# Kernel tuning notes

Hardware: AMD Instinct MI355X
Metric: run time of the kernel (lower is better)

Reference implementation:

```python
import jax, jax.numpy as jnp
import numpy as np

MASK_VALUE = -1000000.0  # matches torch sequence_mask fill value


def setup_inputs() -> dict:
    key = jax.random.key(0)
    k1, k2, k3, k4 = jax.random.split(key, 4)
    B, Tq, Tk, d = 16, 2048, 2048, 128
    queries = jax.random.normal(k1, (B, Tq, d), dtype=jnp.float32)
    keys = jax.random.normal(k2, (B, Tk, d), dtype=jnp.float32)
    values = jax.random.normal(k3, (B, Tk, d), dtype=jnp.float32)
    valid_lens = jax.random.randint(k4, (B, Tq), 0, Tk, dtype=jnp.int64)
    return {"queries": queries, "keys": keys, "values": values,
            "valid_lens": valid_lens}


def reference(queries, keys, values, valid_lens):
    d = queries.shape[-1]
    Tk = keys.shape[1]
    # scores: [B, Tq, Tk]
    scores = jnp.einsum('bqd,bkd->bqk', queries, keys) / jnp.sqrt(
        jnp.asarray(d, dtype=queries.dtype))
    # per-row length mask: position k is valid iff k < valid_lens[b, q]
    mask = jnp.arange(Tk)[None, None, :] < valid_lens[:, :, None]
    scores = jnp.where(mask, scores, jnp.asarray(MASK_VALUE, scores.dtype))
    attn = jax.nn.softmax(scores, axis=-1)
    # dropout p=0.0 -> identity
    return jnp.einsum('bqk,bkd->bqd', attn, values)
```

## Files before the change

kernel.cpp:

```cpp
#include <hip/hip_runtime.h>
#include <stdint.h>
#include <math.h>

#define NB 16
#define TQ 2048
#define TK 2048
#define DH 128
#define KT (TK / 64)
#define QB (TQ / 64)

#define CT   8
#define CTL  3
#define NCH  4
#define NJOBS (NB * QB * NCH)
#define PBLK 768

#define QK_STR 136
#define VT_STR 72
#define P_STR  72

#define SK_OFF 0
#define SV_OFF 17408
#define SP_OFF 35840
#define SM_BYTES 45056

typedef __attribute__((ext_vector_type(8))) short bf16x8;
typedef __attribute__((ext_vector_type(4))) float f32x4;
typedef __attribute__((ext_vector_type(8))) unsigned short u16x8;

__device__ __forceinline__ unsigned short f2b(float f) {
  union { float f; uint32_t u; } v; v.f = f;
  uint32_t u = v.u;
  return (unsigned short)((u + 0x7fffu + ((u >> 16) & 1u)) >> 16);
}

__device__ __forceinline__ u16x8 cvt8(const float* p) {
  const f32x4 a = *(const f32x4*)p;
  const f32x4 b = *(const f32x4*)(p + 4);
  u16x8 o;
#pragma unroll
  for (int j = 0; j < 4; ++j) { o[j] = f2b(a[j]); o[4 + j] = f2b(b[j]); }
  return o;
}

__device__ __forceinline__ int eff_len(const int* vlen, bool is64, int idx) {
  int v = is64 ? vlen[2 * idx] : vlen[idx];
  v = (v < 0) ? 0 : ((v > TK) ? TK : v);
  return (v == 0) ? TK : v;
}

__global__ __launch_bounds__(256) void prep_sort(const float* __restrict__ K,
                                                 const float* __restrict__ V,
                                                 unsigned short* __restrict__ Kb,
                                                 unsigned short* __restrict__ Vt,
                                                 const int* __restrict__ vlen,
                                                 int* __restrict__ perm,
                                                 int* __restrict__ tick) {
  __shared__ alignas(16) char sm[17424];
  const int t = threadIdx.x;
  const int b = blockIdx.y;

  if (blockIdx.x == KT) {
    int* cnt_  = (int*)sm;
    int* base_ = cnt_ + (TK + 1);
    int* psum  = base_ + (TK + 1);

    if (b == 0 && t == 0) tick[0] = 0;

    int hw = 0;
#pragma unroll
    for (int i = 0; i < 8; ++i) hw |= vlen[2 * i + 1];
    const bool is64 = (hw == 0);

    for (int i = t; i <= TK; i += 256) cnt_[i] = 0;
    __syncthreads();

    int eff[8];
#pragma unroll
    for (int j = 0; j < 8; ++j) {
      const int q = j * 256 + t;
      eff[j] = eff_len(vlen, is64, b * TQ + q);
      atomicAdd(&cnt_[eff[j]], 1);
    }
    __syncthreads();

    int loc[8]; int s = 0;
#pragma unroll
    for (int j = 0; j < 8; ++j) { loc[j] = cnt_[TK - (t * 8 + j)]; s += loc[j]; }
    psum[t] = s;
    __syncthreads();
    if (t == 0) {
      int acc = 0;
      for (int i = 0; i < 256; ++i) { const int x = psum[i]; psum[i] = acc; acc += x; }
    }
    __syncthreads();
    int run = psum[t];
#pragma unroll
    for (int j = 0; j < 8; ++j) { base_[TK - (t * 8 + j)] = run; run += loc[j]; }
    __syncthreads();
#pragma unroll
    for (int j = 0; j < 8; ++j) {
      const int rank = atomicAdd(&base_[eff[j]], 1);
      perm[b * TQ + rank] = j * 256 + t;
    }
    return;
  }

  unsigned short (*tile)[136] = (unsigned short (*)[136])sm;
  const int kt = blockIdx.x;
  const int k0 = kt * 64;

  const float* Ks = K + ((size_t)b * TK + k0) * DH;
  unsigned short* Kd = Kb + ((size_t)b * TK + k0) * DH;
#pragma unroll
  for (int i = 0; i < 4; ++i) {
    const int row = i * 16 + (t >> 4);
    const int c0 = (t & 15) * 8;
    *(u16x8*)(Kd + (size_t)row * DH + c0) = cvt8(Ks + (size_t)row * DH + c0);
  }
  const float* Vs = V + ((size_t)b * TK + k0) * DH;
#pragma unroll
  for (int i = 0; i < 4; ++i) {
    const int row = i * 16 + (t >> 4);
    const int c0 = (t & 15) * 8;
    *(u16x8*)(&tile[row][c0]) = cvt8(Vs + (size_t)row * DH + c0);
  }
  __syncthreads();
  {
    const int d = t >> 1;
    const int half = t & 1;
    alignas(16) unsigned short tmp[32];
#pragma unroll
    for (int j = 0; j < 32; ++j) tmp[j] = tile[half * 32 + j][d];
    unsigned short* dst = Vt + ((size_t)(b * KT + kt) * DH + d) * 64 + half * 32;
#pragma unroll
    for (int j = 0; j < 4; ++j)
      *(u16x8*)(dst + j * 8) = *(const u16x8*)(&tmp[j * 8]);
  }
}

__global__ __launch_bounds__(256) void attn_pers(const float* __restrict__ Q,
                                                 const unsigned short* __restrict__ Kp,
                                                 const unsigned short* __restrict__ Vp,
                                                 const int* __restrict__ vlen,
                                                 const int* __restrict__ perm,
                                                 float* __restrict__ pO,
                                                 float* __restrict__ pL,
                                                 float* __restrict__ out,
                                                 int* __restrict__ tick) {
  __shared__ alignas(16) char smem[SM_BYTES];
  __shared__ int s_job;
  unsigned short* sK = (unsigned short*)(smem + SK_OFF);
  unsigned short* sV = (unsigned short*)(smem + SV_OFF);

  const int tid  = threadIdx.x;
  const int w    = tid >> 6;
  const int lane = tid & 63;
  const int quad = lane >> 4;
  const int l15  = lane & 15;
  const int krow = tid >> 4;
  const int kch  = tid & 15;

  int hw = 0;
#pragma unroll
  for (int i = 0; i < 8; ++i) hw |= vlen[2 * i + 1];
  const bool is64 = (hw == 0);

  const float kScaleL2 = 0.08838834764831845f * 1.4426950408889634f;
  const float kBias    = -32.0f;
  const float kKill    = -1.0e7f;

  unsigned short* sP = (unsigned short*)(smem + SP_OFF) + w * (16 * P_STR);

  for (;;) {
    __syncthreads();
    if (tid == 0) s_job = atomicAdd(tick, 1);
    __syncthreads();
    const int job = s_job;
    if (job >= NJOBS) return;

    const int cchunk = job >> 9;
    const int jq     = (job >> 4) & 31;
    const int b      = job & 15;
    const int q0 = jq * 64;
    const int qw = q0 + w * 16;

    const int bvl = eff_len(vlen, is64, b * TQ + perm[b * TQ + q0]);
    const int wvl = eff_len(vlen, is64, b * TQ + perm[b * TQ + qw]);
    const int nt = (bvl + 63) >> 6;
    const int t0 = cchunk * CT;
    const int t1 = (nt < t0 + CT) ? nt : (t0 + CT);
    if (t0 >= t1) continue;
    const int nact = (nt + CT - 1) >> CTL;

    const unsigned short* Kbase = Kp + (size_t)b * TK * DH;
    const unsigned short* Vbase = Vp + (size_t)(b * KT) * DH * 64;

    u16x8 kreg[4], vreg[4];
    {
      const unsigned short* Ksrc = Kbase + (size_t)t0 * 64 * DH;
#pragma unroll
      for (int i = 0; i < 4; ++i)
        kreg[i] = *(const u16x8*)(Ksrc + (size_t)(i * 16 + krow) * DH + kch * 8);
      const unsigned short* Vsrc = Vbase + (size_t)t0 * (DH * 64);
#pragma unroll
      for (int i = 0; i < 4; ++i)
        vreg[i] = *(const u16x8*)(Vsrc + (i * 256 + tid) * 8);
    }

    bf16x8 qa[4];
    {
      const int qmrow = perm[b * TQ + qw + l15];
      const float* qptr = Q + ((size_t)b * TQ + qmrow) * DH + quad * 8;
#pragma unroll
      for (int kc = 0; kc < 4; ++kc) {
        union { u16x8 u; bf16x8 f; } cv;
        cv.u = cvt8(qptr + kc * 32);
        qa[kc] = cv.f;
      }
    }

    int vlr[4]; float scl[4]; int qidx[4];
#pragma unroll
    for (int r = 0; r < 4; ++r) {
      const int rank = qw + quad * 4 + r;
      const int qrow = perm[b * TQ + rank];
      qidx[r] = qrow;
      const int idx = b * TQ + qrow;
      int v = is64 ? vlen[2 * idx] : vlen[idx];
      v = (v < 0) ? 0 : ((v > TK) ? TK : v);
      scl[r] = (v == 0) ? 0.0f : kScaleL2;
      vlr[r] = (v == 0) ? TK : v;
    }

    f32x4 Of[8] = {};
    float l_r[4] = {0.f, 0.f, 0.f, 0.f};

    for (int t = t0; t < t1; ++t) {
#pragma unroll
      for (int i = 0; i < 4; ++i)
        *(u16x8*)(sK + (i * 16 + krow) * QK_STR + kch * 8) = kreg[i];
#pragma unroll
      for (int i = 0; i < 4; ++i) {
        const int chunk = i * 256 + tid;
        *(u16x8*)(sV + (chunk >> 3) * VT_STR + (chunk & 7) * 8) = vreg[i];
      }
      __syncthreads();

      if (t + 1 < t1) {
        const unsigned short* Ksrc = Kbase + (size_t)(t + 1) * 64 * DH;
#pragma unroll
        for (int i = 0; i < 4; ++i)
          kreg[i] = *(const u16x8*)(Ksrc + (size_t)(i * 16 + krow) * DH + kch * 8);
        const unsigned short* Vsrc = Vbase + (size_t)(t + 1) * (DH * 64);
#pragma unroll
        for (int i = 0; i < 4; ++i)
          vreg[i] = *(const u16x8*)(Vsrc + (i * 256 + tid) * 8);
      }

      const int k0 = t * 64;
      if (k0 < wvl) {
        f32x4 sc[4] = {};
#pragma unroll
        for (int ct = 0; ct < 4; ++ct) {
          const unsigned short* kr = sK + (ct * 16 + l15) * QK_STR;
#pragma unroll
          for (int kc = 0; kc < 4; ++kc) {
            const bf16x8 kf = *(const bf16x8*)(kr + (kc * 4 + quad) * 8);
            sc[ct] = __builtin_amdgcn_mfma_f32_16x16x32_bf16(qa[kc], kf, sc[ct], 0, 0, 0);
          }
        }

        unsigned short pb[4][4];
#pragma unroll
        for (int ct = 0; ct < 4; ++ct) {
          const int kpos = k0 + ct * 16 + l15;
#pragma unroll
          for (int r = 0; r < 4; ++r) {
            const float s = (kpos < vlr[r]) ? fmaf(sc[ct][r], scl[r], kBias) : kKill;
            const float p = exp2f(s);
            l_r[r] += p;
            pb[ct][r] = f2b(p);
          }
        }

#pragma unroll
        for (int ct = 0; ct < 4; ++ct)
#pragma unroll
          for (int r = 0; r < 4; ++r)
            sP[(quad * 4 + r) * P_STR + ct * 16 + l15] = pb[ct][r];
        __asm__ __volatile__("" ::: "memory");

        bf16x8 pa[2];
        {
          const unsigned short* pr = sP + l15 * P_STR;
#pragma unroll
          for (int ch = 0; ch < 2; ++ch)
            pa[ch] = *(const bf16x8*)(pr + (ch * 4 + quad) * 8);
        }

#pragma unroll
        for (int dt = 0; dt < 8; ++dt) {
          const unsigned short* vr = sV + (dt * 16 + l15) * VT_STR;
#pragma unroll
          for (int ch = 0; ch < 2; ++ch) {
            const bf16x8 vf = *(const bf16x8*)(vr + (ch * 4 + quad) * 8);
            Of[dt] = __builtin_amdgcn_mfma_f32_16x16x32_bf16(pa[ch], vf, Of[dt], 0, 0, 0);
          }
        }
      }
      __syncthreads();
    }

#pragma unroll
    for (int off = 1; off <= 8; off <<= 1)
#pragma unroll
      for (int r = 0; r < 4; ++r)
        l_r[r] += __shfl_xor(l_r[r], off, 64);

    if (nact == 1) {
#pragma unroll
      for (int r = 0; r < 4; ++r) {
        const float inv = 1.0f / l_r[r];
        float* orow = out + ((size_t)b * TQ + qidx[r]) * DH;
#pragma unroll
        for (int dt = 0; dt < 8; ++dt)
          orow[dt * 16 + l15] = Of[dt][r] * inv;
      }
      continue;
    }

    const int slot = (b * QB + jq) * NCH + cchunk;
    float* po = pO + (size_t)slot * (64 * DH);
    float* pl = pL + (size_t)slot * 64;
#pragma unroll
    for (int r = 0; r < 4; ++r) {
      const int row = w * 16 + quad * 4 + r;
#pragma unroll
      for (int dt = 0; dt < 8; ++dt)
        po[(size_t)row * DH + dt * 16 + l15] = Of[dt][r];
    }
    if (l15 == 0) {
#pragma unroll
      for (int r = 0; r < 4; ++r)
        pl[w * 16 + quad * 4 + r] = l_r[r];
    }
  }
}

__global__ __launch_bounds__(256) void combine_kernel(const float* __restrict__ pO,
                                                      const float* __restrict__ pL,
                                                      const int* __restrict__ perm,
                                                      const int* __restrict__ vlen,
                                                      float* __restrict__ out) {
  const int b = blockIdx.y;
  const int j = blockIdx.x;
  const int t = threadIdx.x;

  int hw = 0;
#pragma unroll
  for (int i = 0; i < 8; ++i) hw |= vlen[2 * i + 1];
  const bool is64 = (hw == 0);

  const int bvl = eff_len(vlen, is64, b * TQ + perm[b * TQ + j * 64]);
  const int nt = (bvl + 63) >> 6;
  const int nact = (nt + CT - 1) >> CTL;
  if (nact <= 1) return;

  const int qboff = (b * QB + j) * NCH;
#pragma unroll
  for (int i = 0; i < 8; ++i) {
    const int u = i * 256 + t;
    const int r = u >> 5;
    const int d4 = (u & 31) * 4;
    float lsum = 0.0f;
    f32x4 acc = {0.f, 0.f, 0.f, 0.f};
    for (int c = 0; c < nact; ++c) {
      lsum += pL[(size_t)(qboff + c) * 64 + r];
      acc += *(const f32x4*)(pO + ((size_t)(qboff + c) * 64 + r) * DH + d4);
    }
    const float inv = 1.0f / lsum;
    const int qi = perm[b * TQ + j * 64 + r];
    *(f32x4*)(out + ((size_t)b * TQ + qi) * DH + d4) = acc * inv;
  }
}

__global__ __launch_bounds__(256) void attn_fb(const float* __restrict__ Q,
                                               const float* __restrict__ Kp,
                                               const float* __restrict__ Vp,
                                               const int* __restrict__ vlen,
                                               float* __restrict__ out) {
  __shared__ alignas(16) char smem[53248];
  __shared__ int s_bvl[4];
  unsigned short* sQ = (unsigned short*)smem;
  unsigned short* sK = (unsigned short*)(smem + 17408);
  unsigned short* sV = (unsigned short*)(smem + 34816);

  const int tid  = threadIdx.x;
  const int w    = tid >> 6;
  const int lane = tid & 63;
  const int quad = lane >> 4;
  const int l15  = lane & 15;
  const int b    = blockIdx.y;
  const int q0   = blockIdx.x * 64;

  const float* Qb = Q + ((size_t)b * TQ + q0) * DH;
#pragma unroll
  for (int i = 0; i < 4; ++i) {
    const int row = i * 16 + (tid >> 4);
    const int c0 = (tid & 15) * 8;
    *(u16x8*)(sQ + row * QK_STR + c0) = cvt8(Qb + (size_t)row * DH + c0);
  }

  int hw = 0;
#pragma unroll
  for (int i = 0; i < 8; ++i) hw |= vlen[2 * i + 1];
  const bool is64 = (hw == 0);

  const float kScaleL2 = 0.08838834764831845f * 1.4426950408889634f;
  const float kBias    = -32.0f;
  const float kKill    = -1.0e7f;

  const int qw = q0 + w * 16;
  int vlr[4];
  float scl[4];
#pragma unroll
  for (int r = 0; r < 4; ++r) {
    const int idx = b * TQ + qw + quad * 4 + r;
    int v = is64 ? vlen[2 * idx] : vlen[idx];
    v = (v < 0) ? 0 : ((v > TK) ? TK : v);
    scl[r] = (v == 0) ? 0.0f : kScaleL2;
    vlr[r] = (v == 0) ? TK : v;
  }
  int wvl = 0;
#pragma unroll
  for (int r = 0; r < 4; ++r) wvl = max(wvl, vlr[r]);
  wvl = max(wvl, __shfl_xor(wvl, 16, 64));
  wvl = max(wvl, __shfl_xor(wvl, 32, 64));
  if (lane == 0) s_bvl[w] = wvl;
  __syncthreads();
  const int bvl = max(max(s_bvl[0], s_bvl[1]), max(s_bvl[2], s_bvl[3]));
  const int nt = (bvl + 63) >> 6;

  bf16x8 qa[4];
  {
    const unsigned short* qrow = sQ + (w * 16 + l15) * QK_STR;
#pragma unroll
    for (int kc = 0; kc < 4; ++kc)
      qa[kc] = *(const bf16x8*)(qrow + (kc * 4 + quad) * 8);
  }
  unsigned short* sP = (unsigned short*)smem + w * (16 * P_STR);

  f32x4 Of[8] = {};
  float l_r[4] = {0.f, 0.f, 0.f, 0.f};

  const float* Kb = Kp + (size_t)b * TK * DH;
  const float* Vb = Vp + (size_t)b * TK * DH;

  for (int t = 0; t < nt; ++t) {
    const int k0 = t * 64;
    __syncthreads();
#pragma unroll
    for (int i = 0; i < 4; ++i) {
      const int row = i * 16 + (tid >> 4);
      const int c0 = (tid & 15) * 8;
      *(u16x8*)(sK + row * QK_STR + c0) = cvt8(Kb + (size_t)(k0 + row) * DH + c0);
    }
#pragma unroll
    for (int i = 0; i < 4; ++i) {
      const int row = i * 16 + (tid >> 4);
      const int c0 = (tid & 15) * 8;
      *(u16x8*)(sV + row * QK_STR + c0) = cvt8(Vb + (size_t)(k0 + row) * DH + c0);
    }
    __syncthreads();
    if (k0 >= wvl) continue;

    f32x4 sc[4] = {};
#pragma unroll
    for (int ct = 0; ct < 4; ++ct) {
      const unsigned short* kr = sK + (ct * 16 + l15) * QK_STR;
#pragma unroll
      for (int kc = 0; kc < 4; ++kc) {
        const bf16x8 kf = *(const bf16x8*)(kr + (kc * 4 + quad) * 8);
        sc[ct] = __builtin_amdgcn_mfma_f32_16x16x32_bf16(qa[kc], kf, sc[ct], 0, 0, 0);
      }
    }
    unsigned short pb[4][4];
#pragma unroll
    for (int ct = 0; ct < 4; ++ct) {
      const int kpos = k0 + ct * 16 + l15;
#pragma unroll
      for (int r = 0; r < 4; ++r) {
        const float s = (kpos < vlr[r]) ? fmaf(sc[ct][r], scl[r], kBias) : kKill;
        const float p = exp2f(s);
        l_r[r] += p;
        pb[ct][r] = f2b(p);
      }
    }
#pragma unroll
    for (int ct = 0; ct < 4; ++ct)
#pragma unroll
      for (int r = 0; r < 4; ++r)
        sP[(quad * 4 + r) * P_STR + ct * 16 + l15] = pb[ct][r];
    __asm__ __volatile__("" ::: "memory");
    bf16x8 pa[2];
    {
      const unsigned short* pr = sP + l15 * P_STR;
#pragma unroll
      for (int ch = 0; ch < 2; ++ch)
        pa[ch] = *(const bf16x8*)(pr + (ch * 4 + quad) * 8);
    }
#pragma unroll
    for (int dt = 0; dt < 8; ++dt) {
      const int col = dt * 16 + l15;
#pragma unroll
      for (int ch = 0; ch < 2; ++ch) {
        bf16x8 vf;
#pragma unroll
        for (int j = 0; j < 8; ++j) {
          const int k = ch * 32 + quad * 8 + j;
          vf[j] = ((const short*)sV)[k * QK_STR + col];
        }
        Of[dt] = __builtin_amdgcn_mfma_f32_16x16x32_bf16(pa[ch], vf, Of[dt], 0, 0, 0);
      }
    }
  }

#pragma unroll
  for (int off = 1; off <= 8; off <<= 1)
#pragma unroll
    for (int r = 0; r < 4; ++r)
      l_r[r] += __shfl_xor(l_r[r], off, 64);

#pragma unroll
  for (int r = 0; r < 4; ++r) {
    const float inv = 1.0f / l_r[r];
    const int q = qw + quad * 4 + r;
    float* orow = out + ((size_t)b * TQ + q) * DH;
#pragma unroll
    for (int dt = 0; dt < 8; ++dt)
      orow[dt * 16 + l15] = Of[dt][r] * inv;
  }
}

extern "C" void kernel_launch(void* const* d_in, const int* in_sizes, int n_in,
                              void* d_out, int out_size, void* d_ws, size_t ws_size,
                              hipStream_t stream) {
  const float* Q = (const float*)d_in[0];
  const float* K = (const float*)d_in[1];
  const float* V = (const float*)d_in[2];
  const int* vl  = (const int*)d_in[3];
  float* out     = (float*)d_out;

  const size_t kb    = (size_t)NB * TK * DH;
  const size_t kvB   = kb * 2 * 2;
  const size_t permB = (size_t)NB * TQ * sizeof(int);
  const size_t tickB = 256;
  const size_t pLB   = (size_t)NB * QB * NCH * 64 * sizeof(float);
  const size_t pOB   = (size_t)NB * QB * NCH * 64 * DH * sizeof(float);

  if (ws_size >= kvB + permB + tickB + pLB + pOB) {
    unsigned short* Kb = (unsigned short*)d_ws;
    unsigned short* Vt = Kb + kb;
    int*   perm = (int*)((char*)d_ws + kvB);
    int*   tick = (int*)((char*)d_ws + kvB + permB);
    float* pL   = (float*)((char*)d_ws + kvB + permB + tickB);
    float* pO   = (float*)((char*)d_ws + kvB + permB + tickB + pLB);
    prep_sort<<<dim3(KT + 1, NB), 256, 0, stream>>>(K, V, Kb, Vt, vl, perm, tick);
    attn_pers<<<dim3(PBLK), 256, 0, stream>>>(Q, Kb, Vt, vl, perm, pO, pL, out, tick);
    combine_kernel<<<dim3(QB, NB), 256, 0, stream>>>(pO, pL, perm, vl, out);
  } else {
    attn_fb<<<dim3(QB, NB), 256, 0, stream>>>(Q, K, V, vl, out);
  }
}
```

Baseline: 180.3 us.

## Process 128 query rows per job so each wave reuses K/V tiles twice

Doubles the query tile per persistent job from 64 to 128 rows, so each wave handles two 16-row groups. Every K and V fragment read from shared memory now feeds two MFMAs, and each staged K/V tile serves twice as many queries, halving global K/V traffic per query. It also adds s_setprio around the MFMA loops, reduces the persistent grid to 512 blocks, and resizes the combine kernel and partial buffers to match. The cost is higher register pressure from doubled accumulators, fewer jobs for load balancing across the sorted variable-length rows, and coarser length skipping within a 128-row block.

```diff
diff --git a/kernel.cpp b/kernel.cpp
--- a/kernel.cpp
+++ b/kernel.cpp
@@ -9,11 +9,13 @@
 #define KT (TK / 64)
 #define QB (TQ / 64)
 
+#define QBLK 128
+#define QBn  (TQ / QBLK)
 #define CT   8
 #define CTL  3
 #define NCH  4
-#define NJOBS (NB * QB * NCH)
-#define PBLK 768
+#define NJOBS (NB * QBn * NCH)
+#define PBLK 512
 
 #define QK_STR 136
 #define VT_STR 72
@@ -22,7 +24,7 @@
 #define SK_OFF 0
 #define SV_OFF 17408
 #define SP_OFF 35840
-#define SM_BYTES 45056
+#define SM_BYTES 54272
 
 typedef __attribute__((ext_vector_type(8))) short bf16x8;
 typedef __attribute__((ext_vector_type(4))) float f32x4;
@@ -170,7 +172,7 @@
   const float kBias    = -32.0f;
   const float kKill    = -1.0e7f;
 
-  unsigned short* sP = (unsigned short*)(smem + SP_OFF) + w * (16 * P_STR);
+  unsigned short* sP = (unsigned short*)(smem + SP_OFF) + w * (32 * P_STR);
 
   for (;;) {
     __syncthreads();
@@ -179,11 +181,11 @@
     const int job = s_job;
     if (job >= NJOBS) return;
 
-    const int cchunk = job >> 9;
-    const int jq     = (job >> 4) & 31;
+    const int cchunk = job >> 8;
+    const int jq     = (job >> 4) & 15;
     const int b      = job & 15;
-    const int q0 = jq * 64;
-    const int qw = q0 + w * 16;
+    const int q0 = jq * QBLK;
+    const int qw = q0 + w * 32;
 
     const int bvl = eff_len(vlen, is64, b * TQ + perm[b * TQ + q0]);
     const int wvl = eff_len(vlen, is64, b * TQ + perm[b * TQ + qw]);
@@ -208,33 +210,34 @@
         vreg[i] = *(const u16x8*)(Vsrc + (i * 256 + tid) * 8);
     }
 
-    bf16x8 qa[4];
-    {
-      const int qmrow = perm[b * TQ + qw + l15];
+    bf16x8 qa[2][4];
+#pragma unroll
+    for (int rh = 0; rh < 2; ++rh) {
+      const int qmrow = perm[b * TQ + qw + rh * 16 + l15];
       const float* qptr = Q + ((size_t)b * TQ + qmrow) * DH + quad * 8;
 #pragma unroll
       for (int kc = 0; kc < 4; ++kc) {
         union { u16x8 u; bf16x8 f; } cv;
         cv.u = cvt8(qptr + kc * 32);
-        qa[kc] = cv.f;
-      }
-    }
-
-    int vlr[4]; float scl[4]; int qidx[4];
-#pragma unroll
-    for (int r = 0; r < 4; ++r) {
-      const int rank = qw + quad * 4 + r;
-      const int qrow = perm[b * TQ + rank];
-      qidx[r] = qrow;
-      const int idx = b * TQ + qrow;
-      int v = is64 ? vlen[2 * idx] : vlen[idx];
-      v = (v < 0) ? 0 : ((v > TK) ? TK : v);
-      scl[r] = (v == 0) ? 0.0f : kScaleL2;
-      vlr[r] = (v == 0) ? TK : v;
-    }
-
-    f32x4 Of[8] = {};
-    float l_r[4] = {0.f, 0.f, 0.f, 0.f};
+        qa[rh][kc] = cv.f;
+      }
+    }
+
+    int vlr[2][4]; float scl[2][4];
+#pragma unroll
+    for (int rh = 0; rh < 2; ++rh)
+#pragma unroll
+      for (int r = 0; r < 4; ++r) {
+        const int rank = qw + rh * 16 + quad * 4 + r;
+        const int idx = b * TQ + perm[b * TQ + rank];
+        int v = is64 ? vlen[2 * idx] : vlen[idx];
+        v = (v < 0) ? 0 : ((v > TK) ? TK : v);
+        scl[rh][r] = (v == 0) ? 0.0f : kScaleL2;
+        vlr[rh][r] = (v == 0) ? TK : v;
+      }
+
+    f32x4 Of[2][8] = {};
+    float l_r[2][4] = {};
 
     for (int t = t0; t < t1; ++t) {
 #pragma unroll
@@ -260,90 +263,108 @@
 
       const int k0 = t * 64;
       if (k0 < wvl) {
-        f32x4 sc[4] = {};
+        f32x4 sc[2][4] = {};
+        __builtin_amdgcn_s_setprio(1);
 #pragma unroll
         for (int ct = 0; ct < 4; ++ct) {
           const unsigned short* kr = sK + (ct * 16 + l15) * QK_STR;
 #pragma unroll
           for (int kc = 0; kc < 4; ++kc) {
             const bf16x8 kf = *(const bf16x8*)(kr + (kc * 4 + quad) * 8);
-            sc[ct] = __builtin_amdgcn_mfma_f32_16x16x32_bf16(qa[kc], kf, sc[ct], 0, 0, 0);
+            sc[0][ct] = __builtin_amdgcn_mfma_f32_16x16x32_bf16(qa[0][kc], kf, sc[0][ct], 0, 0, 0);
+            sc[1][ct] = __builtin_amdgcn_mfma_f32_16x16x32_bf16(qa[1][kc], kf, sc[1][ct], 0, 0, 0);
           }
         }
-
-        unsigned short pb[4][4];
-#pragma unroll
-        for (int ct = 0; ct < 4; ++ct) {
-          const int kpos = k0 + ct * 16 + l15;
-#pragma unroll
-          for (int r = 0; r < 4; ++r) {
-            const float s = (kpos < vlr[r]) ? fmaf(sc[ct][r], scl[r], kBias) : kKill;
-            const float p = exp2f(s);
-            l_r[r] += p;
-            pb[ct][r] = f2b(p);
+        __builtin_amdgcn_s_setprio(0);
+
+#pragma unroll
+        for (int rh = 0; rh < 2; ++rh) {
+          unsigned short pb[4][4];
+#pragma unroll
+          for (int ct = 0; ct < 4; ++ct) {
+            const int kpos = k0 + ct * 16 + l15;
+#pragma unroll
+            for (int r = 0; r < 4; ++r) {
+              const float s = (kpos < vlr[rh][r]) ? fmaf(sc[rh][ct][r], scl[rh][r], kBias) : kKill;
+              const float p = exp2f(s);
+              l_r[rh][r] += p;
+              pb[ct][r] = f2b(p);
+            }
+          }
+#pragma unroll
+          for (int ct = 0; ct < 4; ++ct)
+#pragma unroll
+            for (int r = 0; r < 4; ++r)
+              sP[(rh * 16 + quad * 4 + r) * P_STR + ct * 16 + l15] = pb[ct][r];
+        }
+        __asm__ __volatile__("" ::: "memory");
+
+        bf16x8 pa[2][2];
+#pragma unroll
+        for (int rh = 0; rh < 2; ++rh) {
+          const unsigned short* pr = sP + (rh * 16 + l15) * P_STR;
+#pragma unroll
+          for (int ch = 0; ch < 2; ++ch)
+            pa[rh][ch] = *(const bf16x8*)(pr + (ch * 4 + quad) * 8);
+        }
+
+        __builtin_amdgcn_s_setprio(1);
+#pragma unroll
+        for (int dt = 0; dt < 8; ++dt) {
+          const unsigned short* vr = sV + (dt * 16 + l15) * VT_STR;
+#pragma unroll
+          for (int ch = 0; ch < 2; ++ch) {
+            const bf16x8 vf = *(const bf16x8*)(vr + (ch * 4 + quad) * 8);
+            Of[0][dt] = __builtin_amdgcn_mfma_f32_16x16x32_bf16(pa[0][ch], vf, Of[0][dt], 0, 0, 0);
+            Of[1][dt] = __builtin_amdgcn_mfma_f32_16x16x32_bf16(pa[1][ch], vf, Of[1][dt], 0, 0, 0);
           }
         }
-
-#pragma unroll
-        for (int ct = 0; ct < 4; ++ct)
-#pragma unroll
-          for (int r = 0; r < 4; ++r)
-            sP[(quad * 4 + r) * P_STR + ct * 16 + l15] = pb[ct][r];
-        __asm__ __volatile__("" ::: "memory");
-
-        bf16x8 pa[2];
-        {
-          const unsigned short* pr = sP + l15 * P_STR;
-#pragma unroll
-          for (int ch = 0; ch < 2; ++ch)
-            pa[ch] = *(const bf16x8*)(pr + (ch * 4 + quad) * 8);
+        __builtin_amdgcn_s_setprio(0);
+      }
+      __syncthreads();
+    }
+
+#pragma unroll
+    for (int off = 1; off <= 8; off <<= 1)
+#pragma unroll
+      for (int rh = 0; rh < 2; ++rh)
+#pragma unroll
+        for (int r = 0; r < 4; ++r)
+          l_r[rh][r] += __shfl_xor(l_r[rh][r], off, 64);
+
+    if (nact == 1) {
+#pragma unroll
+      for (int rh = 0; rh < 2; ++rh)
+#pragma unroll
+        for (int r = 0; r < 4; ++r) {
+          const float inv = 1.0f / l_r[rh][r];
+          const int qrow = perm[b * TQ + qw + rh * 16 + quad * 4 + r];
+          float* orow = out + ((size_t)b * TQ + qrow) * DH;
+#pragma unroll
+          for (int dt = 0; dt < 8; ++dt)
+            orow[dt * 16 + l15] = Of[rh][dt][r] * inv;
         }
-
-#pragma unroll
-        for (int dt = 0; dt < 8; ++dt) {
-          const unsigned short* vr = sV + (dt * 16 + l15) * VT_STR;
-#pragma unroll
-          for (int ch = 0; ch < 2; ++ch) {
-            const bf16x8 vf = *(const bf16x8*)(vr + (ch * 4 + quad) * 8);
-            Of[dt] = __builtin_amdgcn_mfma_f32_16x16x32_bf16(pa[ch], vf, Of[dt], 0, 0, 0);
-          }
-        }
-      }
-      __syncthreads();
-    }
-
-#pragma unroll
-    for (int off = 1; off <= 8; off <<= 1)
-#pragma unroll
-      for (int r = 0; r < 4; ++r)
-        l_r[r] += __shfl_xor(l_r[r], off, 64);
-
-    if (nact == 1) {
+      continue;
+    }
+
+    const int slot = (b * QBn + jq) * NCH + cchunk;
+    float* po = pO + (size_t)slot * (QBLK * DH);
+    float* pl = pL + (size_t)slot * QBLK;
+#pragma unroll
+    for (int rh = 0; rh < 2; ++rh)
 #pragma unroll
       for (int r = 0; r < 4; ++r) {
-        const float inv = 1.0f / l_r[r];
-        float* orow = out + ((size_t)b * TQ + qidx[r]) * DH;
+        const int row = w * 32 + rh * 16 + quad * 4 + r;
 #pragma unroll
         for (int dt = 0; dt < 8; ++dt)
-          orow[dt * 16 + l15] = Of[dt][r] * inv;
-      }
-      continue;
-    }
-
-    const int slot = (b * QB + jq) * NCH + cchunk;
-    float* po = pO + (size_t)slot * (64 * DH);
-    float* pl = pL + (size_t)slot * 64;
-#pragma unroll
-    for (int r = 0; r < 4; ++r) {
-      const int row = w * 16 + quad * 4 + r;
-#pragma unroll
-      for (int dt = 0; dt < 8; ++dt)
-        po[(size_t)row * DH + dt * 16 + l15] = Of[dt][r];
-    }
+          po[(size_t)row * DH + dt * 16 + l15] = Of[rh][dt][r];
+      }
     if (l15 == 0) {
 #pragma unroll
-      for (int r = 0; r < 4; ++r)
-        pl[w * 16 + quad * 4 + r] = l_r[r];
+      for (int rh = 0; rh < 2; ++rh)
+#pragma unroll
+        for (int r = 0; r < 4; ++r)
+          pl[w * 32 + rh * 16 + quad * 4 + r] = l_r[rh][r];
     }
   }
 }
@@ -362,25 +383,25 @@
   for (int i = 0; i < 8; ++i) hw |= vlen[2 * i + 1];
   const bool is64 = (hw == 0);
 
-  const int bvl = eff_len(vlen, is64, b * TQ + perm[b * TQ + j * 64]);
+  const int bvl = eff_len(vlen, is64, b * TQ + perm[b * TQ + j * QBLK]);
   const int nt = (bvl + 63) >> 6;
   const int nact = (nt + CT - 1) >> CTL;
   if (nact <= 1) return;
 
-  const int qboff = (b * QB + j) * NCH;
-#pragma unroll
-  for (int i = 0; i < 8; ++i) {
+  const int qboff = (b * QBn + j) * NCH;
+#pragma unroll
+  for (int i = 0; i < 16; ++i) {
     const int u = i * 256 + t;
     const int r = u >> 5;
     const int d4 = (u & 31) * 4;
     float lsum = 0.0f;
     f32x4 acc = {0.f, 0.f, 0.f, 0.f};
     for (int c = 0; c < nact; ++c) {
-      lsum += pL[(size_t)(qboff + c) * 64 + r];
-      acc += *(const f32x4*)(pO + ((size_t)(qboff + c) * 64 + r) * DH + d4);
+      lsum += pL[(size_t)(qboff + c) * QBLK + r];
+      acc += *(const f32x4*)(pO + ((size_t)(qboff + c) * QBLK + r) * DH + d4);
     }
     const float inv = 1.0f / lsum;
-    const int qi = perm[b * TQ + j * 64 + r];
+    const int qi = perm[b * TQ + j * QBLK + r];
     *(f32x4*)(out + ((size_t)b * TQ + qi) * DH + d4) = acc * inv;
   }
 }
@@ -556,8 +577,8 @@
   const size_t kvB   = kb * 2 * 2;
   const size_t permB = (size_t)NB * TQ * sizeof(int);
   const size_t tickB = 256;
-  const size_t pLB   = (size_t)NB * QB * NCH * 64 * sizeof(float);
-  const size_t pOB   = (size_t)NB * QB * NCH * 64 * DH * sizeof(float);
+  const size_t pLB   = (size_t)NB * QBn * NCH * QBLK * sizeof(float);
+  const size_t pOB   = (size_t)NB * QBn * NCH * QBLK * DH * sizeof(float);
 
   if (ws_size >= kvB + permB + tickB + pLB + pOB) {
     unsigned short* Kb = (unsigned short*)d_ws;
@@ -568,7 +589,7 @@
     float* pO   = (float*)((char*)d_ws + kvB + permB + tickB + pLB);
     prep_sort<<<dim3(KT + 1, NB), 256, 0, stream>>>(K, V, Kb, Vt, vl, perm, tick);
     attn_pers<<<dim3(PBLK), 256, 0, stream>>>(Q, Kb, Vt, vl, perm, pO, pL, out, tick);
-    combine_kernel<<<dim3(QB, NB), 256, 0, stream>>>(pO, pL, perm, vl, out);
+    combine_kernel<<<dim3(QBn, NB), 256, 0, stream>>>(pO, pL, perm, vl, out);
   } else {
     attn_fb<<<dim3(QB, NB), 256, 0, stream>>>(Q, K, V, vl, out);
   }
```

Measured after the change: 199.7 us. 1.11x slower.

## Load K/V fragments directly from global memory, dropping LDS staging and barriers

Applied to the files above, without the earlier changes.

The K and V tiles are no longer staged through shared memory with a register prefetch and block-wide barriers. Each wave now reads its MFMA operands straight from global (L2-cached) memory and loops only over its own valid key tiles (t1w), so waves with short lengths exit early instead of idling at barriers. The MFMA sections are wrapped in s_setprio, and the persistent grid grows from 768 to 1024 blocks because the smaller LDS footprint allows more resident blocks. The trade-off is more redundant global and L2 traffic, since all four waves reread the same K/V, and global-load latency is no longer hidden by an explicit prefetch.

```diff
diff --git a/kernel.cpp b/kernel.cpp
--- a/kernel.cpp
+++ b/kernel.cpp
@@ -13,16 +13,10 @@
 #define CTL  3
 #define NCH  4
 #define NJOBS (NB * QB * NCH)
-#define PBLK 768
+#define PBLK 1024
 
 #define QK_STR 136
-#define VT_STR 72
 #define P_STR  72
-
-#define SK_OFF 0
-#define SV_OFF 17408
-#define SP_OFF 35840
-#define SM_BYTES 45056
 
 typedef __attribute__((ext_vector_type(8))) short bf16x8;
 typedef __attribute__((ext_vector_type(4))) float f32x4;
@@ -148,18 +142,14 @@
                                                  float* __restrict__ pL,
                                                  float* __restrict__ out,
                                                  int* __restrict__ tick) {
-  __shared__ alignas(16) char smem[SM_BYTES];
+  __shared__ alignas(16) unsigned short sP_all[4 * 16 * P_STR];
   __shared__ int s_job;
-  unsigned short* sK = (unsigned short*)(smem + SK_OFF);
-  unsigned short* sV = (unsigned short*)(smem + SV_OFF);
 
   const int tid  = threadIdx.x;
   const int w    = tid >> 6;
   const int lane = tid & 63;
   const int quad = lane >> 4;
   const int l15  = lane & 15;
-  const int krow = tid >> 4;
-  const int kch  = tid & 15;
 
   int hw = 0;
 #pragma unroll
@@ -170,7 +160,7 @@
   const float kBias    = -32.0f;
   const float kKill    = -1.0e7f;
 
-  unsigned short* sP = (unsigned short*)(smem + SP_OFF) + w * (16 * P_STR);
+  unsigned short* sP = sP_all + w * (16 * P_STR);
 
   for (;;) {
     __syncthreads();
@@ -186,39 +176,16 @@
     const int qw = q0 + w * 16;
 
     const int bvl = eff_len(vlen, is64, b * TQ + perm[b * TQ + q0]);
-    const int wvl = eff_len(vlen, is64, b * TQ + perm[b * TQ + qw]);
     const int nt = (bvl + 63) >> 6;
     const int t0 = cchunk * CT;
-    const int t1 = (nt < t0 + CT) ? nt : (t0 + CT);
-    if (t0 >= t1) continue;
+    if (t0 >= nt) continue;
     const int nact = (nt + CT - 1) >> CTL;
 
-    const unsigned short* Kbase = Kp + (size_t)b * TK * DH;
-    const unsigned short* Vbase = Vp + (size_t)(b * KT) * DH * 64;
-
-    u16x8 kreg[4], vreg[4];
-    {
-      const unsigned short* Ksrc = Kbase + (size_t)t0 * 64 * DH;
-#pragma unroll
-      for (int i = 0; i < 4; ++i)
-        kreg[i] = *(const u16x8*)(Ksrc + (size_t)(i * 16 + krow) * DH + kch * 8);
-      const unsigned short* Vsrc = Vbase + (size_t)t0 * (DH * 64);
-#pragma unroll
-      for (int i = 0; i < 4; ++i)
-        vreg[i] = *(const u16x8*)(Vsrc + (i * 256 + tid) * 8);
-    }
-
-    bf16x8 qa[4];
-    {
-      const int qmrow = perm[b * TQ + qw + l15];
-      const float* qptr = Q + ((size_t)b * TQ + qmrow) * DH + quad * 8;
-#pragma unroll
-      for (int kc = 0; kc < 4; ++kc) {
-        union { u16x8 u; bf16x8 f; } cv;
-        cv.u = cvt8(qptr + kc * 32);
-        qa[kc] = cv.f;
-      }
-    }
+    const int wvl = eff_len(vlen, is64, b * TQ + perm[b * TQ + qw]);
+    const int ntw = (wvl + 63) >> 6;
+    int t1 = t0 + CT;
+    t1 = (nt < t1) ? nt : t1;
+    const int t1w = (ntw < t1) ? ntw : t1;
 
     int vlr[4]; float scl[4]; int qidx[4];
 #pragma unroll
@@ -233,83 +200,80 @@
       vlr[r] = (v == 0) ? TK : v;
     }
 
+    bf16x8 qa[4];
+    {
+      const int qmrow = perm[b * TQ + qw + l15];
+      const float* qptr = Q + ((size_t)b * TQ + qmrow) * DH + quad * 8;
+#pragma unroll
+      for (int kc = 0; kc < 4; ++kc) {
+        union { u16x8 u; bf16x8 f; } cv;
+        cv.u = cvt8(qptr + kc * 32);
+        qa[kc] = cv.f;
+      }
+    }
+
     f32x4 Of[8] = {};
     float l_r[4] = {0.f, 0.f, 0.f, 0.f};
 
-    for (int t = t0; t < t1; ++t) {
-#pragma unroll
-      for (int i = 0; i < 4; ++i)
-        *(u16x8*)(sK + (i * 16 + krow) * QK_STR + kch * 8) = kreg[i];
-#pragma unroll
-      for (int i = 0; i < 4; ++i) {
-        const int chunk = i * 256 + tid;
-        *(u16x8*)(sV + (chunk >> 3) * VT_STR + (chunk & 7) * 8) = vreg[i];
-      }
-      __syncthreads();
-
-      if (t + 1 < t1) {
-        const unsigned short* Ksrc = Kbase + (size_t)(t + 1) * 64 * DH;
-#pragma unroll
-        for (int i = 0; i < 4; ++i)
-          kreg[i] = *(const u16x8*)(Ksrc + (size_t)(i * 16 + krow) * DH + kch * 8);
-        const unsigned short* Vsrc = Vbase + (size_t)(t + 1) * (DH * 64);
-#pragma unroll
-        for (int i = 0; i < 4; ++i)
-          vreg[i] = *(const u16x8*)(Vsrc + (i * 256 + tid) * 8);
-      }
-
+    const unsigned short* Kbase = Kp + (size_t)b * TK * DH;
+
+    for (int t = t0; t < t1w; ++t) {
       const int k0 = t * 64;
-      if (k0 < wvl) {
-        f32x4 sc[4] = {};
-#pragma unroll
-        for (int ct = 0; ct < 4; ++ct) {
-          const unsigned short* kr = sK + (ct * 16 + l15) * QK_STR;
-#pragma unroll
-          for (int kc = 0; kc < 4; ++kc) {
-            const bf16x8 kf = *(const bf16x8*)(kr + (kc * 4 + quad) * 8);
-            sc[ct] = __builtin_amdgcn_mfma_f32_16x16x32_bf16(qa[kc], kf, sc[ct], 0, 0, 0);
-          }
+      const unsigned short* Kt = Kbase + (size_t)k0 * DH;
+      const unsigned short* Vt_ = Vp + ((size_t)(b * KT + t)) * (DH * 64);
+
+      f32x4 sc[4] = {};
+      __builtin_amdgcn_s_setprio(1);
+#pragma unroll
+      for (int ct = 0; ct < 4; ++ct) {
+        const unsigned short* kr = Kt + (size_t)(ct * 16 + l15) * DH + quad * 8;
+#pragma unroll
+        for (int kc = 0; kc < 4; ++kc) {
+          const bf16x8 kf = *(const bf16x8*)(kr + kc * 32);
+          sc[ct] = __builtin_amdgcn_mfma_f32_16x16x32_bf16(qa[kc], kf, sc[ct], 0, 0, 0);
         }
-
-        unsigned short pb[4][4];
-#pragma unroll
-        for (int ct = 0; ct < 4; ++ct) {
-          const int kpos = k0 + ct * 16 + l15;
-#pragma unroll
-          for (int r = 0; r < 4; ++r) {
-            const float s = (kpos < vlr[r]) ? fmaf(sc[ct][r], scl[r], kBias) : kKill;
-            const float p = exp2f(s);
-            l_r[r] += p;
-            pb[ct][r] = f2b(p);
-          }
+      }
+      __builtin_amdgcn_s_setprio(0);
+
+      unsigned short pb[4][4];
+#pragma unroll
+      for (int ct = 0; ct < 4; ++ct) {
+        const int kpos = k0 + ct * 16 + l15;
+#pragma unroll
+        for (int r = 0; r < 4; ++r) {
+          const float s = (kpos < vlr[r]) ? fmaf(sc[ct][r], scl[r], kBias) : kKill;
+          const float p = exp2f(s);
+          l_r[r] += p;
+          pb[ct][r] = f2b(p);
         }
-
-#pragma unroll
-        for (int ct = 0; ct < 4; ++ct)
-#pragma unroll
-          for (int r = 0; r < 4; ++r)
-            sP[(quad * 4 + r) * P_STR + ct * 16 + l15] = pb[ct][r];
-        __asm__ __volatile__("" ::: "memory");
-
-        bf16x8 pa[2];
-        {
-          const unsigned short* pr = sP + l15 * P_STR;
-#pragma unroll
-          for (int ch = 0; ch < 2; ++ch)
-            pa[ch] = *(const bf16x8*)(pr + (ch * 4 + quad) * 8);
+      }
+
+#pragma unroll
+      for (int ct = 0; ct < 4; ++ct)
+#pragma unroll
+        for (int r = 0; r < 4; ++r)
+          sP[(quad * 4 + r) * P_STR + ct * 16 + l15] = pb[ct][r];
+      __asm__ __volatile__("" ::: "memory");
+
+      bf16x8 pa[2];
+      {
+        const unsigned short* pr = sP + l15 * P_STR;
+#pragma unroll
+        for (int ch = 0; ch < 2; ++ch)
+          pa[ch] = *(const bf16x8*)(pr + (ch * 4 + quad) * 8);
+      }
+
+      __builtin_amdgcn_s_setprio(1);
+#pragma unroll
+      for (int dt = 0; dt < 8; ++dt) {
+        const unsigned short* vr = Vt_ + (size_t)(dt * 16 + l15) * 64 + quad * 8;
+#pragma unroll
+        for (int ch = 0; ch < 2; ++ch) {
+          const bf16x8 vf = *(const bf16x8*)(vr + ch * 32);
+          Of[dt] = __builtin_amdgcn_mfma_f32_16x16x32_bf16(pa[ch], vf, Of[dt], 0, 0, 0);
         }
-
-#pragma unroll
-        for (int dt = 0; dt < 8; ++dt) {
-          const unsigned short* vr = sV + (dt * 16 + l15) * VT_STR;
-#pragma unroll
-          for (int ch = 0; ch < 2; ++ch) {
-            const bf16x8 vf = *(const bf16x8*)(vr + (ch * 4 + quad) * 8);
-            Of[dt] = __builtin_amdgcn_mfma_f32_16x16x32_bf16(pa[ch], vf, Of[dt], 0, 0, 0);
-          }
-        }
-      }
-      __syncthreads();
+      }
+      __builtin_amdgcn_s_setprio(0);
     }
 
 #pragma unroll
```

Measured after the change: 300.1 us. 1.66x slower.
